# Optimization experiments

Hardware: AMD Instinct MI355X
Metric: run time of the kernel (lower is better)

## Reference

```python
import jax, jax.numpy as jnp
import numpy as np

DIM = 1024
HEADS = 16
HEAD_DIM = DIM // HEADS


def setup_inputs() -> dict:
    key = jax.random.key(0)
    ks = jax.random.split(key, 12)
    B, Tq, Tk = 2, 2048, 2048
    inp = {
        "query": jax.random.normal(ks[0], (B, Tq, DIM), jnp.float32),
        "key": jax.random.normal(ks[1], (B, Tk, DIM), jnp.float32),
        "value": jax.random.normal(ks[2], (B, Tk, DIM), jnp.float32),
        "mask": jax.random.randint(ks[3], (B, 1, Tq, Tk), 0, 2, jnp.int32),
        # xavier-uniform projection weights (stored [out,in] like torch), zero biases
        "wq": jax.random.uniform(ks[4], (DIM, DIM), jnp.float32, -1.0, 1.0) * np.sqrt(6.0 / (2 * DIM)),
        "wk": jax.random.uniform(ks[5], (DIM, DIM), jnp.float32, -1.0, 1.0) * np.sqrt(6.0 / (2 * DIM)),
        "wv": jax.random.uniform(ks[6], (DIM, DIM), jnp.float32, -1.0, 1.0) * np.sqrt(6.0 / (2 * DIM)),
        "wo": jax.random.uniform(ks[7], (DIM, DIM), jnp.float32, -1.0, 1.0) * np.sqrt(6.0 / (2 * DIM)),
        "bq": jnp.zeros((DIM,), jnp.float32),
        "bk": jnp.zeros((DIM,), jnp.float32),
        "bv": jnp.zeros((DIM,), jnp.float32),
        "bo": jnp.zeros((DIM,), jnp.float32),
    }
    return inp


def reference(query, key, value, mask, wq, wk, wv, wo, bq, bk, bv, bo):
    B, Tq, C = query.shape
    Tk = key.shape[1]
    scale = 1.0 / np.sqrt(HEAD_DIM)
    # projections (torch Linear: x @ W.T + b) -> [B, H, T, Dh]
    q = (query @ wq.T + bq).reshape(B, Tq, HEADS, HEAD_DIM).transpose(0, 2, 1, 3)
    k = (key @ wk.T + bk).reshape(B, Tk, HEADS, HEAD_DIM).transpose(0, 2, 1, 3)
    v = (value @ wv.T + bv).reshape(B, Tk, HEADS, HEAD_DIM).transpose(0, 2, 1, 3)
    scores = jnp.einsum("bhqd,bhkd->bhqk", q, k) * scale
    scores = jnp.clip(scores, -100.0, 100.0)
    scores = jnp.where(mask == 0, -jnp.inf, scores)
    attn = jax.nn.softmax(scores, axis=-1)  # dropout is identity in eval
    out = jnp.einsum("bhqk,bhkd->bhqd", attn, v)
    out = out.transpose(0, 2, 1, 3).reshape(B, Tq, HEADS * HEAD_DIM)
    return out @ wo.T + bo
```

## Files before the change

### kernel.cpp

```cpp
#include <hip/hip_runtime.h>
#include <hip/hip_bf16.h>
#include <stdint.h>


typedef __bf16 bf16;
typedef __bf16 bf16x4 __attribute__((ext_vector_type(4)));
typedef __bf16 bf16x8 __attribute__((ext_vector_type(8)));
typedef float f32x4 __attribute__((ext_vector_type(4)));
typedef short s16x4 __attribute__((ext_vector_type(4)));

#define MFMA_BF16(a, b, c) __builtin_amdgcn_mfma_f32_16x16x32_bf16((a), (b), (c), 0, 0, 0)

__device__ __forceinline__ f32x4 mfma16(bf16x4 a, bf16x4 b, f32x4 c) {
  return __builtin_amdgcn_mfma_f32_16x16x16bf16_1k(
      __builtin_bit_cast(s16x4, a), __builtin_bit_cast(s16x4, b), c, 0, 0, 0);
}

__device__ __forceinline__ void async_load16(const void* g, void* l) {
  __builtin_amdgcn_global_load_lds((const __attribute__((address_space(1))) void*)g,
                                   (__attribute__((address_space(3))) void*)l, 16, 0, 0);
}

__global__ __launch_bounds__(256) void cvt_f32_bf16(
    const float* __restrict__ s0, const float* __restrict__ s1, const float* __restrict__ s2,
    const float* __restrict__ s3, const float* __restrict__ s4, const float* __restrict__ s5,
    const float* __restrict__ s6,
    bf16* __restrict__ d0, bf16* __restrict__ d1, bf16* __restrict__ d2,
    bf16* __restrict__ d3, bf16* __restrict__ d4, bf16* __restrict__ d5,
    bf16* __restrict__ d6) {
  const int z = blockIdx.y;
  const float* s = (z == 0) ? s0 : (z == 1) ? s1 : (z == 2) ? s2 : (z == 3) ? s3
                   : (z == 4) ? s4 : (z == 5) ? s5 : s6;
  bf16* d = (z == 0) ? d0 : (z == 1) ? d1 : (z == 2) ? d2 : (z == 3) ? d3
            : (z == 4) ? d4 : (z == 5) ? d5 : d6;
  const int n4 = (z < 3) ? (4 * 1024 * 1024 / 4) : (1024 * 1024 / 4);
  const int stride = gridDim.x * 256;
  for (int i = blockIdx.x * 256 + threadIdx.x; i < n4; i += stride) {
    const float4 v = ((const float4*)s)[i];
    bf16x4 o;
    o[0] = (bf16)v.x; o[1] = (bf16)v.y; o[2] = (bf16)v.z; o[3] = (bf16)v.w;
    ((bf16x4*)d)[i] = o;
  }
}

__global__ __launch_bounds__(256) void pack_mask_kernel(const int* __restrict__ mask,
                                                        unsigned long long* __restrict__ bits) {
  const int t = blockIdx.x * 256 + threadIdx.x;
  const int v = mask[t];
  const unsigned long long b = __ballot(v != 0);
  if ((threadIdx.x & 63) == 0) bits[t >> 6] = b;
}

__global__ __launch_bounds__(256) void gemm_bt_bias(
    const bf16* __restrict__ X0, const bf16* __restrict__ X1, const bf16* __restrict__ X2,
    const bf16* __restrict__ W0, const bf16* __restrict__ W1, const bf16* __restrict__ W2,
    const float* __restrict__ Bi0, const float* __restrict__ Bi1, const float* __restrict__ Bi2,
    bf16* __restrict__ O0, bf16* __restrict__ O1, bf16* __restrict__ O2,
    float* __restrict__ OF, int K, int N, int vz, int f32out, float qs) {
  const int z = blockIdx.z;
  const bf16* X   = (z == 0) ? X0  : (z == 1) ? X1  : X2;
  const bf16* W   = (z == 0) ? W0  : (z == 1) ? W1  : W2;
  const float* Bi = (z == 0) ? Bi0 : (z == 1) ? Bi1 : Bi2;
  bf16* O         = (z == 0) ? O0  : (z == 1) ? O1  : O2;

  __shared__ __align__(16) unsigned char smem_raw[34816];
  bf16* As  = (bf16*)smem_raw;
  bf16* Bs  = As + 128 * 64;
  bf16* Tt  = (bf16*)smem_raw;
  float* Tf = (float*)smem_raw;

  const int tid = threadIdx.x;
  const int lane = tid & 63;
  const int w = tid >> 6;
  const int la = lane & 15;
  const int qa = lane >> 4;
  const int m0 = blockIdx.x * 128;
  const int n0 = blockIdx.y * 128;
  const int wm = (w & 1) * 64;
  const int wn = (w >> 1) * 64;

  f32x4 acc[4][4];
  for (int i = 0; i < 4; ++i)
    for (int j = 0; j < 4; ++j) acc[i][j] = (f32x4){0.f, 0.f, 0.f, 0.f};

  for (int k0 = 0; k0 < K; k0 += 64) {
    for (int i = 0; i < 4; ++i) {
      const int cb = i * 256 + w * 64;
      const int c = cb + lane;
      const int row = c >> 3;
      const int cc = (c & 7) * 8;
      async_load16(X + (size_t)(m0 + row) * K + k0 + cc, As + (size_t)cb * 8);
      async_load16(W + (size_t)(n0 + row) * K + k0 + cc, Bs + (size_t)cb * 8);
    }
    __syncthreads();
    for (int kk = 0; kk < 64; kk += 32) {
      bf16x8 af[4], bfr[4];
      for (int mt = 0; mt < 4; ++mt)
        af[mt] = *(const bf16x8*)&As[(wm + mt * 16 + la) * 64 + kk + qa * 8];
      for (int nt = 0; nt < 4; ++nt)
        bfr[nt] = *(const bf16x8*)&Bs[(wn + nt * 16 + la) * 64 + kk + qa * 8];
      for (int mt = 0; mt < 4; ++mt)
        for (int nt = 0; nt < 4; ++nt)
          acc[mt][nt] = MFMA_BF16(af[mt], bfr[nt], acc[mt][nt]);
    }
    __syncthreads();
  }

  if (f32out) {
    for (int pass = 0; pass < 2; ++pass) {
      if ((w & 1) == pass) {
        for (int mt = 0; mt < 4; ++mt)
          for (int nt = 0; nt < 4; ++nt)
            for (int r = 0; r < 4; ++r) {
              const int rl = mt * 16 + qa * 4 + r;
              const int cl = wn + nt * 16 + la;
              Tf[rl * 132 + cl] = acc[mt][nt][r] + Bi[n0 + cl];
            }
      }
      __syncthreads();
      for (int i = 0; i < 8; ++i) {
        const int rl = i * 8 + (tid >> 5);
        const int cl = (tid & 31) * 4;
        const float4 vv = *(const float4*)&Tf[rl * 132 + cl];
        *(float4*)&OF[(size_t)(m0 + pass * 64 + rl) * N + n0 + cl] = vv;
      }
      __syncthreads();
    }
  } else if (z != vz) {
    const float sc = (z == 0) ? qs : 1.0f;
    for (int mt = 0; mt < 4; ++mt)
      for (int nt = 0; nt < 4; ++nt)
        for (int r = 0; r < 4; ++r) {
          const int rl = wm + mt * 16 + qa * 4 + r;
          const int cl = wn + nt * 16 + la;
          Tt[rl * 136 + cl] = (bf16)((acc[mt][nt][r] + Bi[n0 + cl]) * sc);
        }
    __syncthreads();
    for (int i = 0; i < 8; ++i) {
      const int rl = i * 16 + (tid >> 4);
      const int cc = (tid & 15) * 8;
      *(bf16x8*)&O[(size_t)(m0 + rl) * N + n0 + cc] = *(const bf16x8*)&Tt[rl * 136 + cc];
    }
  } else {
    for (int mt = 0; mt < 4; ++mt)
      for (int nt = 0; nt < 4; ++nt)
        for (int r = 0; r < 4; ++r) {
          const int rl = wm + mt * 16 + qa * 4 + r;
          const int cl = wn + nt * 16 + la;
          Tt[cl * 136 + rl] = (bf16)(acc[mt][nt][r] + Bi[n0 + cl]);
        }
    __syncthreads();
    const int bb = m0 >> 11;
    const int k0t = m0 & 2047;
    for (int i = 0; i < 8; ++i) {
      const int cl = i * 16 + (tid >> 4);
      const int rr = (tid & 15) * 8;
      *(bf16x8*)&O[((size_t)(bb * 1024 + n0 + cl)) * 2048 + k0t + rr] =
          *(const bf16x8*)&Tt[cl * 136 + rr];
    }
  }
}

__global__ __launch_bounds__(256, 3) void attn_kernel(
    const bf16* __restrict__ Qp, const bf16* __restrict__ Kp, const bf16* __restrict__ Vt,
    const unsigned long long* __restrict__ mbits, bf16* __restrict__ AO) {
  __shared__ bf16 Kb[2][64 * 64];
  __shared__ bf16 Vb[2][64 * 64];

  const int tid = threadIdx.x;
  const int lane = tid & 63;
  const int w = tid >> 6;
  const int la = lane & 15;
  const int qa = lane >> 4;
  const int la7 = la & 7;
  const int b = blockIdx.y >> 4;
  const int h = blockIdx.y & 15;
  const int q0 = blockIdx.x * 64 + w * 16;

  const size_t kbase = (size_t)(b * 2048) * 1024 + h * 64;
  const size_t vbase = ((size_t)(b * 16 + h) * 64) * 2048;
  const unsigned long long* mrow = mbits + ((size_t)(b * 2048 + q0 + la)) * 32;

  const int cb0 = w * 64;
  const int cb1 = 256 + w * 64;
  const int c0 = cb0 + lane, c1 = cb1 + lane;
  const int r0 = c0 >> 3, j0 = (c0 & 7) ^ (r0 & 7);
  const int r1 = c1 >> 3, j1 = (c1 & 7) ^ (r1 & 7);
  const bf16* kp0 = Kp + kbase + (size_t)r0 * 1024 + j0 * 8;
  const bf16* kp1 = Kp + kbase + (size_t)r1 * 1024 + j1 * 8;
  const bf16* vp0 = Vt + vbase + (size_t)r0 * 2048 + j0 * 8;
  const bf16* vp1 = Vt + vbase + (size_t)r1 * 2048 + j1 * 8;

  bf16x8 qf[2];
  for (int kk = 0; kk < 2; ++kk)
    qf[kk] = *(const bf16x8*)&Qp[(size_t)(b * 2048 + q0 + la) * 1024 + h * 64 + kk * 32 + qa * 8];

  bf16x4 ones4;
  for (int j = 0; j < 4; ++j) ones4[j] = (bf16)1.0f;

  int cofs[4];
#pragma unroll
  for (int nt = 0; nt < 4; ++nt)
    cofs[nt] = (((nt * 2 + (qa >> 1)) ^ la7) * 8) + ((qa & 1) * 4);

  f32x4 oacc[5];
  for (int d = 0; d < 5; ++d) oacc[d] = (f32x4){0.f, 0.f, 0.f, 0.f};

  async_load16(kp0, &Kb[0][cb0 * 8]);
  async_load16(kp1, &Kb[0][cb1 * 8]);
  async_load16(vp0, &Vb[0][cb0 * 8]);
  async_load16(vp1, &Vb[0][cb1 * 8]);
  unsigned long long mv = mrow[0];
  __syncthreads();

  for (int kt = 0; kt < 32; ++kt) {
    const int p = kt & 1;
    const bf16* Kc = Kb[p];
    const bf16* Vc = Vb[p];

    unsigned long long mvn = 0;
    if (kt < 31) {
      bf16* Kn = Kb[p ^ 1];
      bf16* Vn = Vb[p ^ 1];
      kp0 += 64 * 1024; kp1 += 64 * 1024;
      vp0 += 64;        vp1 += 64;
      async_load16(kp0, &Kn[cb0 * 8]);
      async_load16(kp1, &Kn[cb1 * 8]);
      async_load16(vp0, &Vn[cb0 * 8]);
      async_load16(vp1, &Vn[cb1 * 8]);
      mvn = mrow[kt + 1];
    }

    f32x4 s[4];
    for (int nt = 0; nt < 4; ++nt) s[nt] = (f32x4){0.f, 0.f, 0.f, 0.f};
#pragma unroll
    for (int kk = 0; kk < 2; ++kk)
#pragma unroll
      for (int nt = 0; nt < 4; ++nt) {
        const bf16x8 kf = *(const bf16x8*)&Kc[(nt * 16 + la) * 64 + (((kk * 4 + qa) ^ la7) * 8)];
        s[nt] = MFMA_BF16(kf, qf[kk], s[nt]);
      }

    bf16x4 vf[4][4];
#pragma unroll
    for (int dt = 0; dt < 4; ++dt)
#pragma unroll
      for (int nt = 0; nt < 4; ++nt)
        vf[dt][nt] = *(const bf16x4*)&Vc[(dt * 16 + la) * 64 + cofs[nt]];

    const unsigned long long mvs = mv >> (qa * 4);
    const uint32_t mlo = (uint32_t)mvs, mhi = (uint32_t)(mvs >> 32);
    bf16x4 pfr[4];
#pragma unroll
    for (int nt = 0; nt < 4; ++nt) {
      const uint32_t mw = ((nt & 2) ? mhi : mlo) >> ((nt & 1) * 16);
#pragma unroll
      for (int r = 0; r < 4; ++r) {
        const float bitf = (float)((mw >> r) & 1u);
        pfr[nt][r] = (bf16)(bitf * exp2f(s[nt][r]));
      }
    }

#pragma unroll
    for (int nt = 0; nt < 4; ++nt) {
#pragma unroll
      for (int dt = 0; dt < 4; ++dt)
        oacc[dt] = mfma16(vf[dt][nt], pfr[nt], oacc[dt]);
      oacc[4] = mfma16(ones4, pfr[nt], oacc[4]);
    }

    mv = mvn;
    __syncthreads();
  }

  const float rl = 1.0f / oacc[4][0];
  for (int dt = 0; dt < 4; ++dt) {
    bf16x4 o4;
    for (int r = 0; r < 4; ++r) o4[r] = (bf16)(oacc[dt][r] * rl);
    *(bf16x4*)&AO[(size_t)(b * 2048 + q0 + la) * 1024 + h * 64 + dt * 16 + qa * 4] = o4;
  }
}

extern "C" void kernel_launch(void* const* d_in, const int* in_sizes, int n_in,
                              void* d_out, int out_size, void* d_ws, size_t ws_size,
                              hipStream_t stream) {
  const float* q    = (const float*)d_in[0];
  const float* k    = (const float*)d_in[1];
  const float* v    = (const float*)d_in[2];
  const int*   mask = (const int*)d_in[3];
  const float* wq   = (const float*)d_in[4];
  const float* wk   = (const float*)d_in[5];
  const float* wv   = (const float*)d_in[6];
  const float* wo   = (const float*)d_in[7];
  const float* bq   = (const float*)d_in[8];
  const float* bk   = (const float*)d_in[9];
  const float* bv   = (const float*)d_in[10];
  const float* bo   = (const float*)d_in[11];

  const size_t M4 = (size_t)4 * 1024 * 1024, M1 = (size_t)1024 * 1024;
  bf16* qb  = (bf16*)d_ws;
  bf16* kb  = qb + M4;
  bf16* vb  = kb + M4;
  bf16* wqb = vb + M4;
  bf16* wkb = wqb + M1;
  bf16* wvb = wkb + M1;
  bf16* wob = wvb + M1;
  bf16* Qp  = wob + M1;
  bf16* Kp  = Qp + M4;
  bf16* Vt  = Kp + M4;
  unsigned long long* mb = (unsigned long long*)(Vt + M4);
  bf16* AO  = qb;
  float* out = (float*)d_out;

  const float QSCALE = 0.18033688011112042f;

  cvt_f32_bf16<<<dim3(2048, 7), dim3(256), 0, stream>>>(
      q, k, v, wq, wk, wv, wo, qb, kb, vb, wqb, wkb, wvb, wob);
  pack_mask_kernel<<<dim3(8388608 / 256), dim3(256), 0, stream>>>(mask, mb);
  gemm_bt_bias<<<dim3(32, 8, 3), dim3(256), 0, stream>>>(
      qb, kb, vb, wqb, wkb, wvb, bq, bk, bv, Qp, Kp, Vt, nullptr, 1024, 1024, 2, 0, QSCALE);
  attn_kernel<<<dim3(32, 32), dim3(256), 0, stream>>>(Qp, Kp, Vt, mb, AO);
  gemm_bt_bias<<<dim3(32, 8, 1), dim3(256), 0, stream>>>(
      AO, AO, AO, wob, wob, wob, bo, bo, bo, nullptr, nullptr, nullptr, out, 1024, 1024, -1, 1, 1.0f);
}
```

Measured before the change: 300.9 us.

## Pre-pack V projection into MFMA fragment order for 16-byte LDS reads

The V projection epilogue now writes V^T in a tiled layout already arranged in MFMA operand fragment order, one block per (batch, head, key tile). The attention kernel can then fetch V fragments with four 16-byte LDS reads per tile instead of sixteen 8-byte reads, and copies each tile with contiguous global loads. This is meant to cut LDS read instructions and swizzle arithmetic in the attention inner loop. In exchange the projection epilogue does more scattered LDS reads and index math, and the two kernels now share a tightly coupled layout.

```diff
diff --git a/kernel.cpp b/kernel.cpp
--- a/kernel.cpp
+++ b/kernel.cpp
@@ -151,12 +151,26 @@
         }
     __syncthreads();
     const int bb = m0 >> 11;
-    const int k0t = m0 & 2047;
+    const int kt0 = (m0 & 2047) >> 6;
+    const int h0 = n0 >> 6;
     for (int i = 0; i < 8; ++i) {
-      const int cl = i * 16 + (tid >> 4);
-      const int rr = (tid & 15) * 8;
-      *(bf16x8*)&O[((size_t)(bb * 1024 + n0 + cl)) * 2048 + k0t + rr] =
-          *(const bf16x8*)&Tt[cl * 136 + rr];
+      const int gi = i * 256 + tid;
+      const int c = gi & 511;
+      const int ktb = (gi >> 9) & 1;
+      const int hb = gi >> 10;
+      const int dt2 = (c >> 8) & 1;
+      const int ntc = (c >> 6) & 3;
+      const int tq = (c >> 3) & 7;
+      const int qac = tq & 3;
+      const int lac = ((tq >> 2) << 3) + (c & 7);
+      const int clA = hb * 64 + dt2 * 32 + lac;
+      const int rlb = ktb * 64 + ntc * 16 + qac * 4;
+      const bf16x4 lo4 = *(const bf16x4*)&Tt[clA * 136 + rlb];
+      const bf16x4 hi4 = *(const bf16x4*)&Tt[(clA + 16) * 136 + rlb];
+      bf16x8 outc;
+      for (int j = 0; j < 4; ++j) { outc[j] = lo4[j]; outc[j + 4] = hi4[j]; }
+      const size_t g16 = ((size_t)((bb * 16 + h0 + hb) * 32) + kt0 + ktb) * 512 + c;
+      *(bf16x8*)&O[g16 * 8] = outc;
     }
   }
 }
@@ -178,7 +192,6 @@
   const int q0 = blockIdx.x * 64 + w * 16;
 
   const size_t kbase = (size_t)(b * 2048) * 1024 + h * 64;
-  const size_t vbase = ((size_t)(b * 16 + h) * 64) * 2048;
   const unsigned long long* mrow = mbits + ((size_t)(b * 2048 + q0 + la)) * 32;
 
   const int cb0 = w * 64;
@@ -188,8 +201,9 @@
   const int r1 = c1 >> 3, j1 = (c1 & 7) ^ (r1 & 7);
   const bf16* kp0 = Kp + kbase + (size_t)r0 * 1024 + j0 * 8;
   const bf16* kp1 = Kp + kbase + (size_t)r1 * 1024 + j1 * 8;
-  const bf16* vp0 = Vt + vbase + (size_t)r0 * 2048 + j0 * 8;
-  const bf16* vp1 = Vt + vbase + (size_t)r1 * 2048 + j1 * 8;
+  const size_t vbase16 = (size_t)((b * 16 + h) * 32) * 512;
+  const bf16* vp0 = Vt + (vbase16 + c0) * 8;
+  const bf16* vp1 = Vt + (vbase16 + c1) * 8;
 
   bf16x8 qf[2];
   for (int kk = 0; kk < 2; ++kk)
@@ -198,10 +212,7 @@
   bf16x4 ones4;
   for (int j = 0; j < 4; ++j) ones4[j] = (bf16)1.0f;
 
-  int cofs[4];
-#pragma unroll
-  for (int nt = 0; nt < 4; ++nt)
-    cofs[nt] = (((nt * 2 + (qa >> 1)) ^ la7) * 8) + ((qa & 1) * 4);
+  const int vsig = (la & 7) + 8 * (qa + 4 * (la >> 3));
 
   f32x4 oacc[5];
   for (int d = 0; d < 5; ++d) oacc[d] = (f32x4){0.f, 0.f, 0.f, 0.f};
@@ -223,7 +234,7 @@
       bf16* Kn = Kb[p ^ 1];
       bf16* Vn = Vb[p ^ 1];
       kp0 += 64 * 1024; kp1 += 64 * 1024;
-      vp0 += 64;        vp1 += 64;
+      vp0 += 4096;      vp1 += 4096;
       async_load16(kp0, &Kn[cb0 * 8]);
       async_load16(kp1, &Kn[cb1 * 8]);
       async_load16(vp0, &Vn[cb0 * 8]);
@@ -241,12 +252,12 @@
         s[nt] = MFMA_BF16(kf, qf[kk], s[nt]);
       }
 
-    bf16x4 vf[4][4];
-#pragma unroll
-    for (int dt = 0; dt < 4; ++dt)
+    bf16x8 vv[2][4];
+#pragma unroll
+    for (int dt2 = 0; dt2 < 2; ++dt2)
 #pragma unroll
       for (int nt = 0; nt < 4; ++nt)
-        vf[dt][nt] = *(const bf16x4*)&Vc[(dt * 16 + la) * 64 + cofs[nt]];
+        vv[dt2][nt] = *(const bf16x8*)&Vc[((dt2 * 4 + nt) * 64 + vsig) * 8];
 
     const unsigned long long mvs = mv >> (qa * 4);
     const uint32_t mlo = (uint32_t)mvs, mhi = (uint32_t)(mvs >> 32);
@@ -264,8 +275,12 @@
 #pragma unroll
     for (int nt = 0; nt < 4; ++nt) {
 #pragma unroll
-      for (int dt = 0; dt < 4; ++dt)
-        oacc[dt] = mfma16(vf[dt][nt], pfr[nt], oacc[dt]);
+      for (int dt2 = 0; dt2 < 2; ++dt2) {
+        const bf16x4 lo = __builtin_shufflevector(vv[dt2][nt], vv[dt2][nt], 0, 1, 2, 3);
+        const bf16x4 hi = __builtin_shufflevector(vv[dt2][nt], vv[dt2][nt], 4, 5, 6, 7);
+        oacc[2 * dt2]     = mfma16(lo, pfr[nt], oacc[2 * dt2]);
+        oacc[2 * dt2 + 1] = mfma16(hi, pfr[nt], oacc[2 * dt2 + 1]);
+      }
       oacc[4] = mfma16(ones4, pfr[nt], oacc[4]);
     }
 
```

Result: no change. 300.8 us (-0.1%).
